# Optimization experiments

Hardware: AMD Instinct MI355X
Metric: run time of the kernel (lower is better)

Reference implementation:

```python
import jax, jax.numpy as jnp
import numpy as np

N_HEADS = 16

def setup_inputs() -> dict:
    key = jax.random.key(0)
    k1, k2, k3 = jax.random.split(key, 3)
    B, L, D = 2, 2048, 1024
    x = jax.random.normal(k1, (B, L, D), dtype=jnp.float32)
    w_qkv = jax.random.normal(k2, (D, 3 * D), dtype=jnp.float32) * (1.0 / np.sqrt(D))
    w_out = jax.random.normal(k3, (D, D), dtype=jnp.float32) * (1.0 / np.sqrt(D))
    return {"x": x, "w_qkv": w_qkv, "w_out": w_out}

def reference(x, w_qkv, w_out):
    B, L, D = x.shape
    H = N_HEADS
    dh = D // H
    qkv = x @ w_qkv                      # (B, L, 3D)
    q, k, v = jnp.split(qkv, 3, axis=-1)
    # (B, H, L, dh)
    q = q.reshape(B, L, H, dh).transpose(0, 2, 1, 3)
    k = k.reshape(B, L, H, dh).transpose(0, 2, 1, 3)
    v = v.reshape(B, L, H, dh).transpose(0, 2, 1, 3)
    scale = 1.0 / jnp.sqrt(jnp.asarray(dh, x.dtype))
    attn = jnp.einsum('bhqd,bhkd->bhqk', q, k) * scale   # (B, H, L, L)
    causal = jnp.tril(jnp.ones((L, L), dtype=bool))
    attn = jnp.where(causal[None, None], attn, -jnp.inf)
    attn = jax.nn.softmax(attn, axis=-1)
    out = jnp.einsum('bhqk,bhkd->bhqd', attn, v)         # (B, H, L, dh)
    out = out.transpose(0, 2, 1, 3).reshape(B, L, D)
    return out @ w_out
```

## Files before the change

### kernel.cpp

```cpp
#include <hip/hip_runtime.h>

typedef __attribute__((ext_vector_type(4))) float f32x4;
typedef __attribute__((ext_vector_type(16))) float f32x16;
typedef __attribute__((ext_vector_type(8))) __bf16 bf16x8;
typedef __attribute__((ext_vector_type(4))) __bf16 bf16x4;
typedef __attribute__((ext_vector_type(4))) unsigned u32x4;
typedef __attribute__((ext_vector_type(2))) unsigned u32x2;

static __device__ __forceinline__ f32x4 mfma16(bf16x8 a, bf16x8 b, f32x4 c) {
    return __builtin_amdgcn_mfma_f32_16x16x32_bf16(a, b, c, 0, 0, 0);
}
static __device__ __forceinline__ f32x16 mfma32(bf16x8 a, bf16x8 b, f32x16 c) {
    return __builtin_amdgcn_mfma_f32_32x32x16_bf16(a, b, c, 0, 0, 0);
}
static __device__ __forceinline__ unsigned pk_bf16(float a, float b) {
    unsigned lo = __builtin_bit_cast(unsigned short, (__bf16)a);
    unsigned hh = __builtin_bit_cast(unsigned short, (__bf16)b);
    return lo | (hh << 16);
}

#define QSCALE 0.18033688f

__global__ __launch_bounds__(256) void prep_all(const float* __restrict__ x,
                                                __bf16* __restrict__ xb,
                                                const float* __restrict__ wq,
                                                __bf16* __restrict__ wqT,
                                                const float* __restrict__ wo,
                                                __bf16* __restrict__ woT) {
    __shared__ float t[32][33];
    int bid = blockIdx.x, tid = threadIdx.x;
    if (bid < 4096) {
        int i = bid * 256 + tid;
        f32x4 v = ((const f32x4*)x)[i];
        bf16x4 o;
#pragma unroll
        for (int j = 0; j < 4; j++) o[j] = (__bf16)v[j];
        ((bf16x4*)xb)[i] = o;
        return;
    }
    const float* in;
    __bf16* out;
    int R, C, bx, by;
    if (bid < 4096 + 3072) {
        int b2 = bid - 4096;
        in = wq; out = wqT; R = 1024; C = 3072;
        bx = (b2 % 96) * 32; by = (b2 / 96) * 32;
    } else {
        int b2 = bid - 7168;
        in = wo; out = woT; R = 1024; C = 1024;
        bx = (b2 % 32) * 32; by = (b2 / 32) * 32;
    }
    int tx = tid & 31, ty = tid >> 5;
#pragma unroll
    for (int k = 0; k < 32; k += 8)
        t[ty + k][tx] = in[(size_t)(by + ty + k) * C + bx + tx];
    __syncthreads();
#pragma unroll
    for (int k = 0; k < 32; k += 8)
        out[(size_t)(bx + ty + k) * R + by + tx] = (__bf16)t[tx][ty + k];
}

#define BN 128
#define BKG 64

template <int MODE, int BMv>
__global__ __launch_bounds__(256) void gemm_bt(const __bf16* __restrict__ A,
                                               const __bf16* __restrict__ Bt,
                                               int M, int N, int K,
                                               float* __restrict__ Cout,
                                               __bf16* __restrict__ Qf,
                                               __bf16* __restrict__ Kf,
                                               __bf16* __restrict__ Vf) {
    constexpr int nMt = BMv / 32;
    __shared__ __attribute__((aligned(16))) __bf16 As[BMv * BKG];
    __shared__ __attribute__((aligned(16))) __bf16 Bs[BN * BKG];
    int tid = threadIdx.x;
    int wave = tid >> 6, lane = tid & 63;
    int lrow = lane & 15, lgrp = lane >> 4;
    int bid = blockIdx.x;
    int m0, n0;
    if (MODE == 1) {
        constexpr int MHALF = 3072 / BMv / 2;
        int x = bid & 7, j = bid >> 3;
        int mx = x & 1, nx = x >> 1;
        int mi = j >> 3, ni = j & 7;
        m0 = (mx * MHALF + mi) * BMv;
        n0 = (nx * 8 + ni) * BN;
    } else {
        int chunk = gridDim.x >> 3;
        int swz = (bid & 7) * chunk + (bid >> 3);
        int nbx = N >> 7;
        m0 = (swz / nbx) * BMv;
        n0 = (swz % nbx) * BN;
    }
    int wm = (wave >> 1) * (BMv / 2);
    int wn = (wave & 1) * 64;

    f32x4 acc[nMt][4];
#pragma unroll
    for (int i = 0; i < nMt; i++)
#pragma unroll
        for (int j = 0; j < 4; j++) acc[i][j] = (f32x4){0.f, 0.f, 0.f, 0.f};

    int srow = tid >> 3;
    int gch = (tid & 7) ^ (srow & 7);
    const __bf16* aSrc = A + (size_t)(m0 + srow) * K + gch * 8;
    const __bf16* bSrc = Bt + (size_t)(n0 + srow) * K + gch * 8;

    for (int k0 = 0; k0 < K; k0 += BKG) {
#pragma unroll
        for (int c = 0; c < BMv / 32; c++) {
            __builtin_amdgcn_global_load_lds(
                (const __attribute__((address_space(1))) void*)(aSrc + k0 + (size_t)c * 32 * K),
                (__attribute__((address_space(3))) void*)(As + (c * 256 + wave * 64) * 8),
                16, 0, 0);
        }
#pragma unroll
        for (int c = 0; c < 4; c++) {
            __builtin_amdgcn_global_load_lds(
                (const __attribute__((address_space(1))) void*)(bSrc + k0 + (size_t)c * 32 * K),
                (__attribute__((address_space(3))) void*)(Bs + (c * 256 + wave * 64) * 8),
                16, 0, 0);
        }
        __syncthreads();
#pragma unroll
        for (int kk = 0; kk < 2; kk++) {
            bf16x8 af[nMt], bfr[4];
#pragma unroll
            for (int mt = 0; mt < nMt; mt++) {
                int row = wm + mt * 16 + lrow;
                int slot = row * 8 + ((4 * kk + lgrp) ^ (row & 7));
                af[mt] = *(const bf16x8*)(As + slot * 8);
            }
#pragma unroll
            for (int nt = 0; nt < 4; nt++) {
                int row = wn + nt * 16 + lrow;
                int slot = row * 8 + ((4 * kk + lgrp) ^ (row & 7));
                bfr[nt] = *(const bf16x8*)(Bs + slot * 8);
            }
#pragma unroll
            for (int mt = 0; mt < nMt; mt++)
#pragma unroll
                for (int nt = 0; nt < 4; nt++)
                    acc[mt][nt] = mfma16(af[mt], bfr[nt], acc[mt][nt]);
        }
        __syncthreads();
    }

#pragma unroll
    for (int mt = 0; mt < nMt; mt++) {
#pragma unroll
        for (int nt = 0; nt < 4; nt++) {
            int f0 = m0 + wm + mt * 16 + lgrp * 4;
            int t = n0 + wn + nt * 16 + lrow;
            if (MODE == 0) {
                *(f32x4*)(Cout + (size_t)t * M + f0) = acc[mt][nt];
            } else {
                int which = f0 >> 10, hn = f0 & 1023;
                int h = hn >> 6, d0 = hn & 63;
                int b = t >> 11, li = t & 2047;
                int bh = b * 16 + h, c = li >> 5, tl = li & 31;
                size_t bhbase = (size_t)bh * 131072;
                if (which == 2) {
                    int ks = tl >> 4, hv = (tl >> 3) & 1, jv = tl & 7;
                    size_t base =
                        bhbase + ((size_t)(c * 4 + ks * 2 + hv) * 64 + d0) * 8 + jv;
#pragma unroll
                    for (int r = 0; r < 4; r++)
                        Vf[base + (size_t)r * 8] = (__bf16)acc[mt][nt][r];
                } else {
                    int st = d0 >> 4, hv = (d0 >> 3) & 1, j0 = d0 & 7;
                    size_t idx =
                        bhbase + ((size_t)(c * 8 + st * 2 + hv) * 32 + tl) * 8 + j0;
                    bf16x4 pv;
                    if (which == 0) {
#pragma unroll
                        for (int r = 0; r < 4; r++)
                            pv[r] = (__bf16)(acc[mt][nt][r] * QSCALE);
                        *(bf16x4*)(Qf + idx) = pv;
                    } else {
#pragma unroll
                        for (int r = 0; r < 4; r++) pv[r] = (__bf16)acc[mt][nt][r];
                        *(bf16x4*)(Kf + idx) = pv;
                    }
                }
            }
        }
    }
}

template <bool MASKED>
static __device__ __forceinline__ void attn_chunk(
    int c, int ql, int hi, const __bf16* __restrict__ Kp,
    const __bf16* __restrict__ Vp, const bf16x8 (&qf)[4], bf16x8 ones,
    f32x16& o0, f32x16& o1, f32x16& lsa) {
    const __bf16* kb = Kp + ((size_t)c * 8 + hi) * 256 + ql * 8;
    bf16x8 kf[4];
#pragma unroll
    for (int st = 0; st < 4; st++) kf[st] = *(const bf16x8*)(kb + st * 512);
    const __bf16* vb = Vp + ((size_t)c * 4 + hi) * 512 + ql * 8;
    bf16x8 v00 = *(const bf16x8*)(vb);
    bf16x8 v01 = *(const bf16x8*)(vb + 256);
    bf16x8 v10 = *(const bf16x8*)(vb + 1024);
    bf16x8 v11 = *(const bf16x8*)(vb + 1280);

    f32x16 sa;
#pragma unroll
    for (int r = 0; r < 16; r++) sa[r] = 0.f;
#pragma unroll
    for (int st = 0; st < 4; st++) sa = mfma32(kf[st], qf[st], sa);

    float p[16];
#pragma unroll
    for (int r = 0; r < 16; r++) {
        float s = sa[r];
        if (MASKED) {
            int krel = (r & 3) + 8 * (r >> 2) + 4 * hi;
            if (krel > ql) s = -1e30f;
        }
        p[r] = __builtin_amdgcn_exp2f(s);
    }

    unsigned w[8];
#pragma unroll
    for (int i = 0; i < 8; i++) w[i] = pk_bf16(p[2 * i], p[2 * i + 1]);
    u32x2 r02 = __builtin_amdgcn_permlane32_swap(w[0], w[2], false, false);
    u32x2 r13 = __builtin_amdgcn_permlane32_swap(w[1], w[3], false, false);
    u32x2 r46 = __builtin_amdgcn_permlane32_swap(w[4], w[6], false, false);
    u32x2 r57 = __builtin_amdgcn_permlane32_swap(w[5], w[7], false, false);
    bf16x8 pa0 = __builtin_bit_cast(bf16x8, (u32x4){r02[0], r13[0], r02[1], r13[1]});
    bf16x8 pa1 = __builtin_bit_cast(bf16x8, (u32x4){r46[0], r57[0], r46[1], r57[1]});

    o0 = mfma32(pa0, v00, o0);
    o1 = mfma32(pa0, v01, o1);
    lsa = mfma32(pa0, ones, lsa);
    o0 = mfma32(pa1, v10, o0);
    o1 = mfma32(pa1, v11, o1);
    lsa = mfma32(pa1, ones, lsa);
}

__global__ __launch_bounds__(256, 4) void attn_fwd13(const __bf16* __restrict__ Qf,
                                                     const __bf16* __restrict__ Kf,
                                                     const __bf16* __restrict__ Vf,
                                                     __bf16* __restrict__ Ob) {
    __shared__ float comb[2][64][49];
    int tid = threadIdx.x;
    int wave = tid >> 6, lane = tid & 63;
    int ql = lane & 31, hi = lane >> 5;
    int bid = blockIdx.x;
    int xcd = bid & 7, idx = bid >> 3;
    int bh = xcd * 4 + (idx >> 6);
    int strip = 63 - (idx & 63);
    int q0 = strip * 32;

    const __bf16* Qp = Qf + (size_t)bh * 131072;
    const __bf16* Kp = Kf + (size_t)bh * 131072;
    const __bf16* Vp = Vf + (size_t)bh * 131072;

    const __bf16* qb = Qp + ((size_t)strip * 8 + hi) * 256 + ql * 8;
    bf16x8 qf[4];
#pragma unroll
    for (int st = 0; st < 4; st++) qf[st] = *(const bf16x8*)(qb + st * 512);

    bf16x8 ones;
#pragma unroll
    for (int j = 0; j < 8; j++) ones[j] = (__bf16)1.0f;

    f32x16 o0, o1, lsa;
#pragma unroll
    for (int r = 0; r < 16; r++) { o0[r] = 0.f; o1[r] = 0.f; lsa[r] = 0.f; }

    for (int c = wave; c < strip; c += 4)
        attn_chunk<false>(c, ql, hi, Kp, Vp, qf, ones, o0, o1, lsa);
    if ((strip & 3) == wave)
        attn_chunk<true>(strip, ql, hi, Kp, Vp, qf, ones, o0, o1, lsa);

    if (wave >= 2) {
        float* sl = &comb[wave - 2][lane][0];
#pragma unroll
        for (int r = 0; r < 16; r++) {
            sl[r] = o0[r]; sl[16 + r] = o1[r]; sl[32 + r] = lsa[r];
        }
    }
    __syncthreads();
    if (wave < 2) {
        const float* sl = &comb[wave][lane][0];
#pragma unroll
        for (int r = 0; r < 16; r++) {
            o0[r] += sl[r]; o1[r] += sl[16 + r]; lsa[r] += sl[32 + r];
        }
    }
    __syncthreads();
    if (wave == 1) {
        float* sl = &comb[0][lane][0];
#pragma unroll
        for (int r = 0; r < 16; r++) {
            sl[r] = o0[r]; sl[16 + r] = o1[r]; sl[32 + r] = lsa[r];
        }
    }
    __syncthreads();
    if (wave == 0) {
        const float* sl = &comb[0][lane][0];
#pragma unroll
        for (int r = 0; r < 16; r++) {
            o0[r] += sl[r]; o1[r] += sl[16 + r]; lsa[r] += sl[32 + r];
        }
        int b = bh >> 4, h = bh & 15;
#pragma unroll
        for (int r = 0; r < 16; r++) {
            int crow = (r & 3) + 8 * (r >> 2) + 4 * hi;
            float inv;
            asm("v_rcp_f32 %0, %1" : "=v"(inv) : "v"(lsa[r]));
            size_t base = ((size_t)(b * 2048 + q0 + crow)) * 1024 + h * 64;
            Ob[base + ql] = (__bf16)(o0[r] * inv);
            Ob[base + 32 + ql] = (__bf16)(o1[r] * inv);
        }
    }
}

extern "C" void kernel_launch(void* const* d_in, const int* in_sizes, int n_in,
                              void* d_out, int out_size, void* d_ws, size_t ws_size,
                              hipStream_t stream) {
    const float* x = (const float*)d_in[0];
    const float* w_qkv = (const float*)d_in[1];
    const float* w_out = (const float*)d_in[2];
    float* out = (float*)d_out;

    char* ws = (char*)d_ws;
    __bf16* xb    = (__bf16*)(ws);
    __bf16* wqkvT = (__bf16*)(ws + (size_t)(8  << 20));
    __bf16* woutT = (__bf16*)(ws + (size_t)(14 << 20));
    __bf16* Qf    = (__bf16*)(ws + (size_t)(16 << 20));
    __bf16* Kf    = (__bf16*)(ws + (size_t)(24 << 20));
    __bf16* Vf    = (__bf16*)(ws + (size_t)(32 << 20));
    __bf16* Ob    = (__bf16*)(ws + (size_t)(40 << 20));

    prep_all<<<8192, 256, 0, stream>>>(x, xb, w_qkv, wqkvT, w_out, woutT);
    gemm_bt<1, 128><<<768, 256, 0, stream>>>(
        wqkvT, xb, 3072, 4096, 1024, nullptr, Qf, Kf, Vf);
    attn_fwd13<<<2048, 256, 0, stream>>>(Qf, Kf, Vf, Ob);
    gemm_bt<0, 64><<<512, 256, 0, stream>>>(
        woutT, Ob, 1024, 4096, 1024, out, nullptr, nullptr, nullptr);
}
```

Baseline: 95.68 us.

## Replace QKV GEMM with 256x256-tile, 8-wave, multi-stage pipelined kernel

Adds a dedicated QKV projection kernel that uses 256x256 output tiles, 512 threads and a 128KB double-buffered LDS ring split into k-halves. Global-to-LDS loads are issued asynchronously with explicit vmcnt waits and barriers, interleaved with MFMA phases at raised priority. The aim is to overlap memory transfer with compute and raise arithmetic intensity over the older 128x128 gemm_bt path. The trade-off is only 192 blocks, which may leave CUs underfilled, plus many barriers per k-step. The generic GEMM loses its QKV mode.

After: 94.83 us. No clear change (-0.9%).

```diff
diff --git a/kernel.cpp b/kernel.cpp
--- a/kernel.cpp
+++ b/kernel.cpp
@@ -20,6 +20,13 @@
 }
 
 #define QSCALE 0.18033688f
+#define FENCE() asm volatile("" ::: "memory")
+#define SYNCB()                          \
+    do {                                 \
+        FENCE();                         \
+        __builtin_amdgcn_s_barrier();    \
+        FENCE();                         \
+    } while (0)
 
 __global__ __launch_bounds__(256) void prep_all(const float* __restrict__ x,
                                                 __bf16* __restrict__ xb,
@@ -60,6 +67,143 @@
         out[(size_t)(bx + ty + k) * R + by + tx] = (__bf16)t[tx][ty + k];
 }
 
+__global__ __launch_bounds__(512, 2) void qkv_gemm8(const __bf16* __restrict__ A,
+                                                    const __bf16* __restrict__ Bt,
+                                                    __bf16* __restrict__ Qf,
+                                                    __bf16* __restrict__ Kf,
+                                                    __bf16* __restrict__ Vf) {
+    const int K = 1024, NT = 16, MT = 12;
+    __shared__ __attribute__((aligned(16))) __bf16 smem[65536];
+    int tid = threadIdx.x;
+    int w = tid >> 6, lane = tid & 63;
+    int lrow = lane & 15, lgrp = lane >> 4;
+    int wm = w >> 2, wn = w & 3;
+    int bid = blockIdx.x;
+    int swz = (bid & 7) * 24 + (bid >> 3);
+    int m0 = (swz % MT) * 256, n0 = (swz / MT) * 256;
+
+    int schunk = ((lane & 3) ^ ((lane >> 3) & 3)) * 8;
+    const __bf16* aS[2];
+    const __bf16* bS[2];
+    int dstRow[2];
+#pragma unroll
+    for (int l = 0; l < 2; l++) {
+        int r = w * 32 + l * 16 + (lane >> 2);
+        aS[l] = A + (size_t)(m0 + r) * K + schunk;
+        bS[l] = Bt + (size_t)(n0 + r) * K + schunk;
+        dstRow[l] = (w * 32 + l * 16) * 64;
+    }
+
+    auto STAGE = [&](int h, int tt) {
+        int tc = tt < NT ? tt : NT - 1;
+        int op = h & 1, kh = h >> 1;
+        int base = ((tt & 1) << 16) + (kh << 15) + (op << 14);
+#pragma unroll
+        for (int l = 0; l < 2; l++) {
+            const __bf16* src = (op ? bS[l] : aS[l]) + tc * 64 + kh * 32;
+            __builtin_amdgcn_global_load_lds(
+                (const __attribute__((address_space(1))) void*)src,
+                (__attribute__((address_space(3))) void*)(smem +
+                                                          ((base + dstRow[l]) >> 1)),
+                16, 0, 0);
+        }
+    };
+
+    int swzsel = (lgrp ^ ((lrow >> 1) & 3)) << 4;
+    auto RDA = [&](int buf, int kk, int row) {
+        int off = (buf << 16) + (kk << 15) + row * 64 + swzsel;
+        return *(const bf16x8*)(smem + (off >> 1));
+    };
+    auto RDB = [&](int buf, int kk, int row) {
+        int off = (buf << 16) + (kk << 15) + 16384 + row * 64 + swzsel;
+        return *(const bf16x8*)(smem + (off >> 1));
+    };
+
+    f32x4 acc[8][4];
+#pragma unroll
+    for (int i = 0; i < 8; i++)
+#pragma unroll
+        for (int j = 0; j < 4; j++) acc[i][j] = (f32x4){0.f, 0.f, 0.f, 0.f};
+    bf16x8 bfr[4];
+
+    STAGE(0, 0); STAGE(1, 0); STAGE(2, 0); STAGE(3, 0);
+    STAGE(0, 1); STAGE(1, 1);
+    asm volatile("s_waitcnt vmcnt(8)" ::: "memory");
+    SYNCB();
+
+#define PH(T, KKv, MHv, SH, ST, DOVM)                                          \
+    {                                                                          \
+        bf16x8 af[4];                                                          \
+        if (MHv == 0) {                                                        \
+            _Pragma("unroll") for (int nt = 0; nt < 4; nt++) bfr[nt] =         \
+                RDB((T) & 1, KKv, wn * 64 + nt * 16 + lrow);                   \
+        }                                                                      \
+        _Pragma("unroll") for (int i = 0; i < 4; i++) af[i] =                  \
+            RDA((T) & 1, KKv, wm * 128 + (MHv * 4 + i) * 16 + lrow);           \
+        STAGE(SH, ST);                                                         \
+        if (DOVM) asm volatile("s_waitcnt vmcnt(8)" ::: "memory");             \
+        SYNCB();                                                               \
+        asm volatile("s_waitcnt lgkmcnt(0)" ::: "memory");                     \
+        __builtin_amdgcn_sched_barrier(0);                                     \
+        __builtin_amdgcn_s_setprio(1);                                         \
+        _Pragma("unroll") for (int i = 0; i < 4; i++)                          \
+            _Pragma("unroll") for (int nt = 0; nt < 4; nt++)                   \
+                acc[MHv * 4 + i][nt] =                                         \
+                    mfma16(af[i], bfr[nt], acc[MHv * 4 + i][nt]);              \
+        __builtin_amdgcn_s_setprio(0);                                         \
+        SYNCB();                                                               \
+    }
+
+#pragma unroll 2
+    for (int t = 0; t < NT; ++t) {
+        PH(t, 0, 0, 2, t + 1, 0);
+        PH(t, 0, 1, 3, t + 1, 1);
+        PH(t, 1, 0, 0, t + 2, 0);
+        PH(t, 1, 1, 1, t + 2, 1);
+    }
+#undef PH
+
+    asm volatile("s_waitcnt vmcnt(0)" ::: "memory");
+    SYNCB();
+
+#pragma unroll
+    for (int mt = 0; mt < 8; mt++) {
+#pragma unroll
+        for (int nt = 0; nt < 4; nt++) {
+            int f0 = m0 + wm * 128 + mt * 16 + lgrp * 4;
+            int t = n0 + wn * 64 + nt * 16 + lrow;
+            int which = f0 >> 10, hn = f0 & 1023;
+            int h = hn >> 6, d0 = hn & 63;
+            int b = t >> 11, li = t & 2047;
+            int bh = b * 16 + h, c = li >> 5, tl = li & 31;
+            size_t bhbase = (size_t)bh * 131072;
+            if (which == 2) {
+                int ks = tl >> 4, hv = (tl >> 3) & 1, jv = tl & 7;
+                size_t base =
+                    bhbase + ((size_t)(c * 4 + ks * 2 + hv) * 64 + d0) * 8 + jv;
+#pragma unroll
+                for (int r = 0; r < 4; r++)
+                    Vf[base + (size_t)r * 8] = (__bf16)acc[mt][nt][r];
+            } else {
+                int st = d0 >> 4, hv = (d0 >> 3) & 1, j0 = d0 & 7;
+                size_t idx =
+                    bhbase + ((size_t)(c * 8 + st * 2 + hv) * 32 + tl) * 8 + j0;
+                bf16x4 pv;
+                if (which == 0) {
+#pragma unroll
+                    for (int r = 0; r < 4; r++)
+                        pv[r] = (__bf16)(acc[mt][nt][r] * QSCALE);
+                    *(bf16x4*)(Qf + idx) = pv;
+                } else {
+#pragma unroll
+                    for (int r = 0; r < 4; r++) pv[r] = (__bf16)acc[mt][nt][r];
+                    *(bf16x4*)(Kf + idx) = pv;
+                }
+            }
+        }
+    }
+}
+
 #define BN 128
 #define BKG 64
 
@@ -67,10 +211,7 @@
 __global__ __launch_bounds__(256) void gemm_bt(const __bf16* __restrict__ A,
                                                const __bf16* __restrict__ Bt,
                                                int M, int N, int K,
-                                               float* __restrict__ Cout,
-                                               __bf16* __restrict__ Qf,
-                                               __bf16* __restrict__ Kf,
-                                               __bf16* __restrict__ Vf) {
+                                               float* __restrict__ Cout) {
     constexpr int nMt = BMv / 32;
     __shared__ __attribute__((aligned(16))) __bf16 As[BMv * BKG];
     __shared__ __attribute__((aligned(16))) __bf16 Bs[BN * BKG];
@@ -78,21 +219,11 @@
     int wave = tid >> 6, lane = tid & 63;
     int lrow = lane & 15, lgrp = lane >> 4;
     int bid = blockIdx.x;
-    int m0, n0;
-    if (MODE == 1) {
-        constexpr int MHALF = 3072 / BMv / 2;
-        int x = bid & 7, j = bid >> 3;
-        int mx = x & 1, nx = x >> 1;
-        int mi = j >> 3, ni = j & 7;
-        m0 = (mx * MHALF + mi) * BMv;
-        n0 = (nx * 8 + ni) * BN;
-    } else {
-        int chunk = gridDim.x >> 3;
-        int swz = (bid & 7) * chunk + (bid >> 3);
-        int nbx = N >> 7;
-        m0 = (swz / nbx) * BMv;
-        n0 = (swz % nbx) * BN;
-    }
+    int chunk = gridDim.x >> 3;
+    int swz = (bid & 7) * chunk + (bid >> 3);
+    int nbx = N >> 7;
+    int m0 = (swz / nbx) * BMv;
+    int n0 = (swz % nbx) * BN;
     int wm = (wave >> 1) * (BMv / 2);
     int wn = (wave & 1) * 64;
 
@@ -153,38 +284,7 @@
         for (int nt = 0; nt < 4; nt++) {
             int f0 = m0 + wm + mt * 16 + lgrp * 4;
             int t = n0 + wn + nt * 16 + lrow;
-            if (MODE == 0) {
-                *(f32x4*)(Cout + (size_t)t * M + f0) = acc[mt][nt];
-            } else {
-                int which = f0 >> 10, hn = f0 & 1023;
-                int h = hn >> 6, d0 = hn & 63;
-                int b = t >> 11, li = t & 2047;
-                int bh = b * 16 + h, c = li >> 5, tl = li & 31;
-                size_t bhbase = (size_t)bh * 131072;
-                if (which == 2) {
-                    int ks = tl >> 4, hv = (tl >> 3) & 1, jv = tl & 7;
-                    size_t base =
-                        bhbase + ((size_t)(c * 4 + ks * 2 + hv) * 64 + d0) * 8 + jv;
-#pragma unroll
-                    for (int r = 0; r < 4; r++)
-                        Vf[base + (size_t)r * 8] = (__bf16)acc[mt][nt][r];
-                } else {
-                    int st = d0 >> 4, hv = (d0 >> 3) & 1, j0 = d0 & 7;
-                    size_t idx =
-                        bhbase + ((size_t)(c * 8 + st * 2 + hv) * 32 + tl) * 8 + j0;
-                    bf16x4 pv;
-                    if (which == 0) {
-#pragma unroll
-                        for (int r = 0; r < 4; r++)
-                            pv[r] = (__bf16)(acc[mt][nt][r] * QSCALE);
-                        *(bf16x4*)(Qf + idx) = pv;
-                    } else {
-#pragma unroll
-                        for (int r = 0; r < 4; r++) pv[r] = (__bf16)acc[mt][nt][r];
-                        *(bf16x4*)(Kf + idx) = pv;
-                    }
-                }
-            }
+            *(f32x4*)(Cout + (size_t)t * M + f0) = acc[mt][nt];
         }
     }
 }
@@ -336,9 +436,8 @@
     __bf16* Ob    = (__bf16*)(ws + (size_t)(40 << 20));
 
     prep_all<<<8192, 256, 0, stream>>>(x, xb, w_qkv, wqkvT, w_out, woutT);
-    gemm_bt<1, 128><<<768, 256, 0, stream>>>(
-        wqkvT, xb, 3072, 4096, 1024, nullptr, Qf, Kf, Vf);
+    qkv_gemm8<<<192, 512, 0, stream>>>(wqkvT, xb, Qf, Kf, Vf);
     attn_fwd13<<<2048, 256, 0, stream>>>(Qf, Kf, Vf, Ob);
     gemm_bt<0, 64><<<512, 256, 0, stream>>>(
-        woutT, Ob, 1024, 4096, 1024, out, nullptr, nullptr, nullptr);
-}
+        woutT, Ob, 1024, 4096, 1024, out);
+}
```
